# Kernel optimization log

Measured on AMD Instinct MI355X. Metric: run time of the kernel, lower is better.

## Reference

```python
import jax, jax.numpy as jnp
import numpy as np

N, E, G, D = 100000, 400000, 4000, 128
AF, BF, L = 74, 12, 11  # atom/bond feat sizes; L = n_layers-1 GNN layers after GetContext


def _p(k, shape, fan):
    return jax.random.normal(k, shape, dtype=jnp.float32) * (fan ** -0.5)


def setup_inputs() -> dict:
    key = jax.random.key(0)
    ks = iter(jax.random.split(key, 32))
    z = lambda *s: jnp.zeros(s, jnp.float32)
    return dict(
        atom_feats=jax.random.normal(next(ks), (N, AF), jnp.float32),
        bond_feats=jax.random.normal(next(ks), (E, BF), jnp.float32),
        src=jax.random.randint(next(ks), (E,), 0, N, jnp.int32),
        dst=jax.random.randint(next(ks), (E,), 0, N, jnp.int32),
        node_graph_ids=jnp.sort(jax.random.randint(next(ks), (N,), 0, G, jnp.int32)),
        W_node=_p(next(ks), (AF, D), AF), b_node=z(D),
        W_edge1=_p(next(ks), (AF + BF, D), AF + BF), b_edge1=z(D),
        W_edge2=_p(next(ks), (2 * D, 1), 2 * D), b_edge2=z(1),
        W_et=_p(next(ks), (D, D), D), b_et=z(D),
        gru0_Wih=_p(next(ks), (3 * D, D), D), gru0_bih=z(3 * D),
        gru0_Whh=_p(next(ks), (3 * D, D), D), gru0_bhh=z(3 * D),
        Wpe=_p(next(ks), (L, 2 * D, 1), 2 * D), bpe=z(L, 1),
        Wpn=_p(next(ks), (L, D, D), D), bpn=z(L, D),
        gru_Wih=_p(next(ks), (L, 3 * D, D), D), gru_bih=z(L, 3 * D),
        gru_Whh=_p(next(ks), (L, 3 * D, D), D), gru_bhh=z(L, 3 * D),
        Wr1=_p(next(ks), (D, D), D), br1=z(D),
        Wr2=_p(next(ks), (D, D), D), br2=z(D),
    )


def leaky_relu(x):
    return jnp.where(x > 0, x, 0.01 * x)


def edge_softmax(logits, dst):
    # softmax of edge logits grouped by destination node (DGL edge_softmax)
    m = jax.ops.segment_max(logits, dst, num_segments=N)
    m = jnp.where(jnp.isfinite(m), m, 0.0)
    e = jnp.exp(logits - m[dst])
    s = jax.ops.segment_sum(e, dst, num_segments=N)
    return e / s[dst]


def gru_cell(x, h, Wih, bih, Whh, bhh):
    gi = x @ Wih.T + bih
    gh = h @ Whh.T + bhh
    ir, iz, ig = jnp.split(gi, 3, axis=-1)
    hr, hz, hg = jnp.split(gh, 3, axis=-1)
    r = jax.nn.sigmoid(ir + hr)
    z = jax.nn.sigmoid(iz + hz)
    n = jnp.tanh(ig + r * hg)
    return (1.0 - z) * n + z * h


def _attentive_fp(atom_feats, bond_feats, src, dst, node_graph_ids,
                  W_node, b_node, W_edge1, b_edge1, W_edge2, b_edge2,
                  W_et, b_et, gru0_Wih, gru0_bih, gru0_Whh, gru0_bhh,
                  Wpe, bpe, Wpn, bpn, gru_Wih, gru_bih, gru_Whh, gru_bhh,
                  Wr1, br1, Wr2, br2):
    # --- GetContext (dropout = identity at inference) ---
    hv_new = leaky_relu(atom_feats @ W_node + b_node)                       # [N,D]
    he1 = leaky_relu(jnp.concatenate([atom_feats[src], bond_feats], 1) @ W_edge1 + b_edge1)  # [E,D]
    logits = leaky_relu(jnp.concatenate([hv_new[dst], he1], 1) @ W_edge2 + b_edge2)          # [E,1]
    a = edge_softmax(logits, dst)
    c = jax.ops.segment_sum(a * (he1 @ W_et + b_et), dst, num_segments=N)   # [N,D]
    h = jax.nn.relu(gru_cell(jax.nn.elu(c), hv_new, gru0_Wih, gru0_bih, gru0_Whh, gru0_bhh))

    # --- 11 GNNLayers (AttentiveGRU2) via scan over stacked params ---
    def layer(h, p):
        Wpe_l, bpe_l, Wpn_l, bpn_l, Wih, bih, Whh, bhh = p
        lg = leaky_relu(jnp.concatenate([h[dst], h[src]], 1) @ Wpe_l + bpe_l)  # [E,1]
        a = edge_softmax(lg, dst)
        hp = h @ Wpn_l + bpn_l
        c = jax.ops.segment_sum(hp[src] * a, dst, num_segments=N)
        return jax.nn.relu(gru_cell(jax.nn.elu(c), h, Wih, bih, Whh, bhh)), None

    h, _ = jax.lax.scan(layer, h, (Wpe, bpe, Wpn, bpn, gru_Wih, gru_bih, gru_Whh, gru_bhh))

    # --- MLPNodeReadout, mode='mean' ---
    x = jax.nn.relu(h @ Wr1 + br1) @ Wr2 + br2
    sums = jax.ops.segment_sum(x, node_graph_ids, num_segments=G)
    counts = jax.ops.segment_sum(jnp.ones((N, 1), x.dtype), node_graph_ids, num_segments=G)
    return sums / jnp.maximum(counts, 1.0)                                  # [G,D]


def reference(atom_feats, bond_feats, src, dst, node_graph_ids,
              W_node, b_node, W_edge1, b_edge1, W_edge2, b_edge2,
              W_et, b_et, gru0_Wih, gru0_bih, gru0_Whh, gru0_bhh,
              Wpe, bpe, Wpn, bpn, gru_Wih, gru_bih, gru_Whh, gru_bhh,
              Wr1, br1, Wr2, br2):
    return _attentive_fp(atom_feats, bond_feats, src, dst, node_graph_ids,
                         W_node, b_node, W_edge1, b_edge1, W_edge2, b_edge2,
                         W_et, b_et, gru0_Wih, gru0_bih, gru0_Whh, gru0_bhh,
                         Wpe, bpe, Wpn, bpn, gru_Wih, gru_bih, gru_Whh, gru_bhh,
                         Wr1, br1, Wr2, br2)
```

## Files before the change

### kernel.cpp

```cpp
#include <hip/hip_runtime.h>
#include <cstdio>
#include <cstddef>

enum { ACT_NONE = 0, ACT_LEAKY = 1, ACT_RELU = 2 };

typedef __attribute__((ext_vector_type(8))) short short8v;
typedef __attribute__((ext_vector_type(4))) float f32x4;

__device__ __forceinline__ float leakyf(float x) { return x > 0.f ? x : 0.01f * x; }

__device__ __forceinline__ unsigned fenc(float f) {
    unsigned u = __float_as_uint(f);
    return (u & 0x80000000u) ? ~u : (u | 0x80000000u);
}
__device__ __forceinline__ float fdec(unsigned u) {
    return (u & 0x80000000u) ? __uint_as_float(u & 0x7FFFFFFFu) : __uint_as_float(~u);
}

__device__ __forceinline__ unsigned bf16rtn(float x) {
    unsigned u = __float_as_uint(x);
    return (u + 0x7FFFu + ((u >> 16) & 1u)) >> 16;
}
__device__ __forceinline__ void split8(float4 a, float4 b, short8v& hi, short8v& lo) {
    const float v[8] = {a.x, a.y, a.z, a.w, b.x, b.y, b.z, b.w};
#pragma unroll
    for (int i = 0; i < 8; i++) {
        const unsigned hb = bf16rtn(v[i]);
        const float r = v[i] - __uint_as_float(hb << 16);
        hi[i] = (short)hb;
        lo[i] = (short)bf16rtn(r);
    }
}

__global__ __launch_bounds__(256) void wsplit_k(
    const float* __restrict__ Wih, const float* __restrict__ Whh,
    unsigned short* __restrict__ whi, unsigned short* __restrict__ wlo)
{
    const int i4 = (blockIdx.x * 256 + threadIdx.x) * 4;
    if (i4 >= 98304) return;
    const float* src = (i4 < 49152) ? (Wih + i4) : (Whh + (i4 - 49152));
    const float4 v = *(const float4*)src;
    const float vv[4] = {v.x, v.y, v.z, v.w};
    unsigned short h4[4], l4[4];
#pragma unroll
    for (int i = 0; i < 4; i++) {
        const unsigned hb = bf16rtn(vv[i]);
        const float r = vv[i] - __uint_as_float(hb << 16);
        h4[i] = (unsigned short)hb;
        l4[i] = (unsigned short)bf16rtn(r);
    }
    *(ushort4*)&whi[i4] = make_ushort4(h4[0], h4[1], h4[2], h4[3]);
    *(ushort4*)&wlo[i4] = make_ushort4(l4[0], l4[1], l4[2], l4[3]);
}

__global__ __launch_bounds__(256) void wsplitT_k(
    const float* __restrict__ W,
    unsigned short* __restrict__ whi, unsigned short* __restrict__ wlo)
{
    const int idx = blockIdx.x * 256 + threadIdx.x;
    if (idx >= 16384) return;
    const int k = idx >> 7, col = idx & 127;
    const float v = W[idx];
    const unsigned hb = bf16rtn(v);
    const float r = v - __uint_as_float(hb << 16);
    whi[col * 128 + k] = (unsigned short)hb;
    wlo[col * 128 + k] = (unsigned short)bf16rtn(r);
}

__global__ __launch_bounds__(256) void wsplitT96_k(
    const float* __restrict__ W,
    unsigned short* __restrict__ whi, unsigned short* __restrict__ wlo, int K)
{
    const int idx = blockIdx.x * 256 + threadIdx.x;
    if (idx >= 12288) return;
    const int col = idx / 96, k = idx - col * 96;
    const float v = (k < K) ? W[(size_t)k * 128 + col] : 0.f;
    const unsigned hb = bf16rtn(v);
    const float r = v - __uint_as_float(hb << 16);
    whi[idx] = (unsigned short)hb;
    wlo[idx] = (unsigned short)bf16rtn(r);
}

__global__ __launch_bounds__(512) void gru_fused_mfma_k(
    const float* __restrict__ cbuf, const unsigned short* __restrict__ whi,
    const unsigned short* __restrict__ wlo, const float* __restrict__ bih,
    const float* __restrict__ bhh, float* __restrict__ h,
    const float* __restrict__ wa, const float* __restrict__ wb,
    float* __restrict__ pd, float* __restrict__ ps,
    const unsigned short* __restrict__ w3hi, const unsigned short* __restrict__ w3lo,
    const float* __restrict__ b3, float* __restrict__ out3, int act3, int M)
{
    __shared__ __align__(16) char smem[64 * 132 * 4];
    short (*lhi)[4][64][8] = (short(*)[4][64][8])smem;
    short (*llo)[4][64][8] = (short(*)[4][64][8])(smem + 16384);
    float (*fbuf)[132] = (float(*)[132])smem;

    const int t    = threadIdx.x;
    const int lane = t & 63;
    const int w    = t >> 6;
    const int rBase = blockIdx.x * 64;

    const int sRS = t >> 3, sQ = t & 7;
    const int sRow = rBase + sRS;
    const int sRT = sRS >> 4, sLrow = sRS & 15;

    auto stage = [&](const float* __restrict__ A, bool doElu) {
#pragma unroll
        for (int half = 0; half < 2; half++) {
            const int k0 = sQ * 16 + half * 8;
            const int kc = k0 >> 5;
            const int g  = (k0 & 31) >> 3;
            float4 f0 = make_float4(0.f, 0.f, 0.f, 0.f);
            float4 f1 = make_float4(0.f, 0.f, 0.f, 0.f);
            if (sRow < M) {
                f0 = *(const float4*)&A[(size_t)sRow * 128 + k0];
                f1 = *(const float4*)&A[(size_t)sRow * 128 + k0 + 4];
                if (doElu) {
                    f0.x = f0.x > 0.f ? f0.x : expm1f(f0.x);
                    f0.y = f0.y > 0.f ? f0.y : expm1f(f0.y);
                    f0.z = f0.z > 0.f ? f0.z : expm1f(f0.z);
                    f0.w = f0.w > 0.f ? f0.w : expm1f(f0.w);
                    f1.x = f1.x > 0.f ? f1.x : expm1f(f1.x);
                    f1.y = f1.y > 0.f ? f1.y : expm1f(f1.y);
                    f1.z = f1.z > 0.f ? f1.z : expm1f(f1.z);
                    f1.w = f1.w > 0.f ? f1.w : expm1f(f1.w);
                }
            }
            short8v h8, l8;
            split8(f0, f1, h8, l8);
            *(short8v*)&lhi[sRT][kc][sLrow + g * 16][0] = h8;
            *(short8v*)&llo[sRT][kc][sLrow + g * 16][0] = l8;
        }
    };

    f32x4 accr[4], accz[4], accig[4], acchg[4];
#pragma unroll
    for (int rt = 0; rt < 4; rt++) {
        accr[rt]  = (f32x4){0.f, 0.f, 0.f, 0.f};
        accz[rt]  = (f32x4){0.f, 0.f, 0.f, 0.f};
        accig[rt] = (f32x4){0.f, 0.f, 0.f, 0.f};
        acchg[rt] = (f32x4){0.f, 0.f, 0.f, 0.f};
    }

    const int cw   = w * 16 + (lane & 15);
    const int koff = (lane >> 4) * 8;

    stage(cbuf, true);
    __syncthreads();
#pragma unroll
    for (int kc = 0; kc < 4; kc++) {
        short8v bh[3], bl[3];
#pragma unroll
        for (int g = 0; g < 3; g++) {
            const size_t off = (size_t)(g * 128 + cw) * 128 + kc * 32 + koff;
            bh[g] = *(const short8v*)&whi[off];
            bl[g] = *(const short8v*)&wlo[off];
        }
#pragma unroll
        for (int rt = 0; rt < 4; rt++) {
            const short8v ah = *(const short8v*)&lhi[rt][kc][lane][0];
            const short8v al = *(const short8v*)&llo[rt][kc][lane][0];
            accr[rt]  = __builtin_amdgcn_mfma_f32_16x16x32_bf16(ah, bh[0], accr[rt], 0, 0, 0);
            accr[rt]  = __builtin_amdgcn_mfma_f32_16x16x32_bf16(al, bh[0], accr[rt], 0, 0, 0);
            accr[rt]  = __builtin_amdgcn_mfma_f32_16x16x32_bf16(ah, bl[0], accr[rt], 0, 0, 0);
            accz[rt]  = __builtin_amdgcn_mfma_f32_16x16x32_bf16(ah, bh[1], accz[rt], 0, 0, 0);
            accz[rt]  = __builtin_amdgcn_mfma_f32_16x16x32_bf16(al, bh[1], accz[rt], 0, 0, 0);
            accz[rt]  = __builtin_amdgcn_mfma_f32_16x16x32_bf16(ah, bl[1], accz[rt], 0, 0, 0);
            accig[rt] = __builtin_amdgcn_mfma_f32_16x16x32_bf16(ah, bh[2], accig[rt], 0, 0, 0);
            accig[rt] = __builtin_amdgcn_mfma_f32_16x16x32_bf16(al, bh[2], accig[rt], 0, 0, 0);
            accig[rt] = __builtin_amdgcn_mfma_f32_16x16x32_bf16(ah, bl[2], accig[rt], 0, 0, 0);
        }
    }
    __syncthreads();

    stage(h, false);
    __syncthreads();
#pragma unroll
    for (int kc = 0; kc < 4; kc++) {
        short8v bh[3], bl[3];
#pragma unroll
        for (int g = 0; g < 3; g++) {
            const size_t off = (size_t)(384 + g * 128 + cw) * 128 + kc * 32 + koff;
            bh[g] = *(const short8v*)&whi[off];
            bl[g] = *(const short8v*)&wlo[off];
        }
#pragma unroll
        for (int rt = 0; rt < 4; rt++) {
            const short8v ah = *(const short8v*)&lhi[rt][kc][lane][0];
            const short8v al = *(const short8v*)&llo[rt][kc][lane][0];
            accr[rt]  = __builtin_amdgcn_mfma_f32_16x16x32_bf16(ah, bh[0], accr[rt], 0, 0, 0);
            accr[rt]  = __builtin_amdgcn_mfma_f32_16x16x32_bf16(al, bh[0], accr[rt], 0, 0, 0);
            accr[rt]  = __builtin_amdgcn_mfma_f32_16x16x32_bf16(ah, bl[0], accr[rt], 0, 0, 0);
            accz[rt]  = __builtin_amdgcn_mfma_f32_16x16x32_bf16(ah, bh[1], accz[rt], 0, 0, 0);
            accz[rt]  = __builtin_amdgcn_mfma_f32_16x16x32_bf16(al, bh[1], accz[rt], 0, 0, 0);
            accz[rt]  = __builtin_amdgcn_mfma_f32_16x16x32_bf16(ah, bl[1], accz[rt], 0, 0, 0);
            acchg[rt] = __builtin_amdgcn_mfma_f32_16x16x32_bf16(ah, bh[2], acchg[rt], 0, 0, 0);
            acchg[rt] = __builtin_amdgcn_mfma_f32_16x16x32_bf16(al, bh[2], acchg[rt], 0, 0, 0);
            acchg[rt] = __builtin_amdgcn_mfma_f32_16x16x32_bf16(ah, bl[2], acchg[rt], 0, 0, 0);
        }
    }

    const bool post = (wa != nullptr) || (w3hi != nullptr);
    const float br_  = bih[cw] + bhh[cw];
    const float bz_  = bih[128 + cw] + bhh[128 + cw];
    const float big_ = bih[256 + cw];
    const float bhg_ = bhh[256 + cw];
    if (post) __syncthreads();
#pragma unroll
    for (int rt = 0; rt < 4; rt++) {
        const int lr0 = rt * 16 + ((lane >> 4) << 2);
#pragma unroll
        for (int i = 0; i < 4; i++) {
            const int row = rBase + lr0 + i;
            const bool ok = (row < M);
            float hnew = 0.f;
            if (ok) {
                const float hv = h[(size_t)row * 128 + cw];
                const float r  = 1.f / (1.f + expf(-(accr[rt][i] + br_)));
                const float z  = 1.f / (1.f + expf(-(accz[rt][i] + bz_)));
                const float nn = tanhf(accig[rt][i] + big_ + r * (acchg[rt][i] + bhg_));
                hnew = fmaxf((1.f - z) * nn + z * hv, 0.f);
                h[(size_t)row * 128 + cw] = hnew;
            }
            if (post) fbuf[lr0 + i][cw] = hnew;
        }
    }
    if (!post) return;
    __syncthreads();

    if (wa && t < 64 && rBase + t < M) {
        float accd = 0.f, accs = 0.f;
        for (int cc = 0; cc < 128; cc++) {
            const float hv = fbuf[t][cc];
            accd = fmaf(hv, wa[cc], accd);
            accs = fmaf(hv, wb[cc], accs);
        }
        pd[rBase + t] = accd;
        ps[rBase + t] = accs;
    }

    if (w3hi) {
        float4 rv[2][2];
#pragma unroll
        for (int half = 0; half < 2; half++) {
            const int k0 = sQ * 16 + half * 8;
            rv[half][0] = *(const float4*)&fbuf[sRS][k0];
            rv[half][1] = *(const float4*)&fbuf[sRS][k0 + 4];
        }
        __syncthreads();
#pragma unroll
        for (int half = 0; half < 2; half++) {
            const int k0 = sQ * 16 + half * 8;
            const int kc = k0 >> 5;
            const int g  = (k0 & 31) >> 3;
            short8v h8, l8;
            split8(rv[half][0], rv[half][1], h8, l8);
            *(short8v*)&lhi[sRT][kc][sLrow + g * 16][0] = h8;
            *(short8v*)&llo[sRT][kc][sLrow + g * 16][0] = l8;
        }
        __syncthreads();

        f32x4 acc3[4];
#pragma unroll
        for (int rt = 0; rt < 4; rt++) acc3[rt] = (f32x4){0.f, 0.f, 0.f, 0.f};
#pragma unroll
        for (int kc = 0; kc < 4; kc++) {
            const size_t off = (size_t)cw * 128 + kc * 32 + koff;
            const short8v bh = *(const short8v*)&w3hi[off];
            const short8v bl = *(const short8v*)&w3lo[off];
#pragma unroll
            for (int rt = 0; rt < 4; rt++) {
                const short8v ah = *(const short8v*)&lhi[rt][kc][lane][0];
                const short8v al = *(const short8v*)&llo[rt][kc][lane][0];
                acc3[rt] = __builtin_amdgcn_mfma_f32_16x16x32_bf16(ah, bh, acc3[rt], 0, 0, 0);
                acc3[rt] = __builtin_amdgcn_mfma_f32_16x16x32_bf16(al, bh, acc3[rt], 0, 0, 0);
                acc3[rt] = __builtin_amdgcn_mfma_f32_16x16x32_bf16(ah, bl, acc3[rt], 0, 0, 0);
            }
        }
        const float b0 = b3[cw];
#pragma unroll
        for (int rt = 0; rt < 4; rt++) {
            const int r0 = rBase + rt * 16 + ((lane >> 4) << 2);
#pragma unroll
            for (int i = 0; i < 4; i++) {
                const int row = r0 + i;
                if (row >= M) continue;
                float v = acc3[rt][i] + b0;
                if (act3 == ACT_LEAKY)      v = v > 0.f ? v : 0.01f * v;
                else if (act3 == ACT_RELU)  v = fmaxf(v, 0.f);
                out3[(size_t)row * 128 + cw] = v;
            }
        }
    }
}

__global__ __launch_bounds__(512) void mfma128_k(
    const float* __restrict__ A, const unsigned short* __restrict__ whi,
    const unsigned short* __restrict__ wlo, const float* __restrict__ bias,
    float* __restrict__ C, int M, int actOut)
{
    __shared__ short lhi[4][4][64][8];
    __shared__ short llo[4][4][64][8];
    const int t    = threadIdx.x;
    const int lane = t & 63;
    const int w    = t >> 6;
    const int rBase = blockIdx.x * 64;

    {
        const int rS = t >> 3, q = t & 7;
        const int row = rBase + rS;
        const int rt = rS >> 4, lrow = rS & 15;
#pragma unroll
        for (int half = 0; half < 2; half++) {
            const int k0 = q * 16 + half * 8;
            const int kc = k0 >> 5;
            const int g  = (k0 & 31) >> 3;
            float4 f0 = make_float4(0.f, 0.f, 0.f, 0.f);
            float4 f1 = make_float4(0.f, 0.f, 0.f, 0.f);
            if (row < M) {
                f0 = *(const float4*)&A[(size_t)row * 128 + k0];
                f1 = *(const float4*)&A[(size_t)row * 128 + k0 + 4];
            }
            short8v h8, l8;
            split8(f0, f1, h8, l8);
            *(short8v*)&lhi[rt][kc][lrow + g * 16][0] = h8;
            *(short8v*)&llo[rt][kc][lrow + g * 16][0] = l8;
        }
    }
    __syncthreads();

    f32x4 acc[4];
#pragma unroll
    for (int rt = 0; rt < 4; rt++) acc[rt] = (f32x4){0.f, 0.f, 0.f, 0.f};

    const int cw   = w * 16 + (lane & 15);
    const int koff = (lane >> 4) * 8;

#pragma unroll
    for (int kc = 0; kc < 4; kc++) {
        const size_t off = (size_t)cw * 128 + kc * 32 + koff;
        const short8v bh = *(const short8v*)&whi[off];
        const short8v bl = *(const short8v*)&wlo[off];
#pragma unroll
        for (int rt = 0; rt < 4; rt++) {
            const short8v ah = *(const short8v*)&lhi[rt][kc][lane][0];
            const short8v al = *(const short8v*)&llo[rt][kc][lane][0];
            acc[rt] = __builtin_amdgcn_mfma_f32_16x16x32_bf16(ah, bh, acc[rt], 0, 0, 0);
            acc[rt] = __builtin_amdgcn_mfma_f32_16x16x32_bf16(al, bh, acc[rt], 0, 0, 0);
            acc[rt] = __builtin_amdgcn_mfma_f32_16x16x32_bf16(ah, bl, acc[rt], 0, 0, 0);
        }
    }

    const float b0 = bias[cw];
#pragma unroll
    for (int rt = 0; rt < 4; rt++) {
        const int r0 = rBase + rt * 16 + ((lane >> 4) << 2);
#pragma unroll
        for (int i = 0; i < 4; i++) {
            const int row = r0 + i;
            if (row >= M) continue;
            float v = acc[rt][i] + b0;
            if (actOut == ACT_LEAKY)      v = v > 0.f ? v : 0.01f * v;
            else if (actOut == ACT_RELU)  v = fmaxf(v, 0.f);
            C[(size_t)row * 128 + cw] = v;
        }
    }
}

__global__ __launch_bounds__(512) void mfma96_k(
    const float* __restrict__ A1, const float* __restrict__ A2,
    const int* __restrict__ idx,
    const unsigned short* __restrict__ whi, const unsigned short* __restrict__ wlo,
    const float* __restrict__ bias, float* __restrict__ C,
    const float* __restrict__ dotW, float* __restrict__ dotOut,
    int writeC, int M, int K1, int actOut)
{
    __shared__ __align__(16) char smem[64 * 130 * 4];
    short (*lhi)[3][64][8] = (short(*)[3][64][8])smem;
    short (*llo)[3][64][8] = (short(*)[3][64][8])(smem + 12288);
    float (*fbuf)[130] = (float(*)[130])smem;

    const int t    = threadIdx.x;
    const int lane = t & 63;
    const int w    = t >> 6;
    const int rBase = blockIdx.x * 64;

    {
        const int rS = t >> 3, q = t & 7;
        const int row = rBase + rS;
        const int rt = rS >> 4, lrow = rS & 15;
#pragma unroll
        for (int half = 0; half < 2; half++) {
            const int k0 = q * 16 + half * 8;
            if (k0 >= 96) continue;
            const int kc = k0 >> 5;
            const int g  = (k0 & 31) >> 3;
            float v[8] = {0.f, 0.f, 0.f, 0.f, 0.f, 0.f, 0.f, 0.f};
            if (row < M) {
                const int ar = idx ? idx[row] : row;
                const float* __restrict__ a1 = A1 + (size_t)ar * K1;
#pragma unroll
                for (int j = 0; j < 8; j++) {
                    const int k = k0 + j;
                    if (k < K1)                 v[j] = a1[k];
                    else if (A2 && k < K1 + 12) v[j] = A2[(size_t)row * 12 + (k - K1)];
                }
            }
            short8v h8, l8;
            split8(make_float4(v[0], v[1], v[2], v[3]),
                   make_float4(v[4], v[5], v[6], v[7]), h8, l8);
            *(short8v*)&lhi[rt][kc][lrow + g * 16][0] = h8;
            *(short8v*)&llo[rt][kc][lrow + g * 16][0] = l8;
        }
    }
    __syncthreads();

    f32x4 acc[4];
#pragma unroll
    for (int rt = 0; rt < 4; rt++) acc[rt] = (f32x4){0.f, 0.f, 0.f, 0.f};

    const int cw   = w * 16 + (lane & 15);
    const int koff = (lane >> 4) * 8;

#pragma unroll
    for (int kc = 0; kc < 3; kc++) {
        const size_t off = (size_t)cw * 96 + kc * 32 + koff;
        const short8v bh = *(const short8v*)&whi[off];
        const short8v bl = *(const short8v*)&wlo[off];
#pragma unroll
        for (int rt = 0; rt < 4; rt++) {
            const short8v ah = *(const short8v*)&lhi[rt][kc][lane][0];
            const short8v al = *(const short8v*)&llo[rt][kc][lane][0];
            acc[rt] = __builtin_amdgcn_mfma_f32_16x16x32_bf16(ah, bh, acc[rt], 0, 0, 0);
            acc[rt] = __builtin_amdgcn_mfma_f32_16x16x32_bf16(al, bh, acc[rt], 0, 0, 0);
            acc[rt] = __builtin_amdgcn_mfma_f32_16x16x32_bf16(ah, bl, acc[rt], 0, 0, 0);
        }
    }

    const float b0 = bias[cw];
    if (dotOut) __syncthreads();
#pragma unroll
    for (int rt = 0; rt < 4; rt++) {
        const int lr0 = rt * 16 + ((lane >> 4) << 2);
#pragma unroll
        for (int i = 0; i < 4; i++) {
            const int row = rBase + lr0 + i;
            const bool ok = (row < M);
            float v = acc[rt][i] + b0;
            if (actOut == ACT_LEAKY)      v = v > 0.f ? v : 0.01f * v;
            else if (actOut == ACT_RELU)  v = fmaxf(v, 0.f);
            if (ok && writeC) C[(size_t)row * 128 + cw] = v;
            if (dotOut) fbuf[lr0 + i][cw] = ok ? v : 0.f;
        }
    }
    if (dotOut) {
        __syncthreads();
        if (t < 64 && rBase + t < M) {
            float accd = 0.f;
            for (int cc = 0; cc < 128; cc++)
                accd = fmaf(fbuf[t][cc], dotW[cc], accd);
            dotOut[rBase + t] = accd;
        }
    }
}

__global__ __launch_bounds__(256) void edge_lgc_k(
    const float* __restrict__ pd, const float* __restrict__ pe,
    const float* __restrict__ b2, const int* __restrict__ dst,
    float* __restrict__ lg, unsigned* __restrict__ m_u, int E)
{
    const int e = blockIdx.x * blockDim.x + threadIdx.x;
    if (e >= E) return;
    const int d = dst[e];
    const float v = leakyf(pd[d] + pe[e] + b2[0]);
    lg[e] = v;
    atomicMax(&m_u[d], fenc(v));
}

__global__ __launch_bounds__(256) void edge_exp_k(
    float* __restrict__ lg, const unsigned* __restrict__ m_u,
    float* __restrict__ s, const int* __restrict__ dst, int E)
{
    const int e = blockIdx.x * blockDim.x + threadIdx.x;
    if (e >= E) return;
    const int d = dst[e];
    const float ex = expf(lg[e] - fdec(m_u[d]));
    lg[e] = ex;
    atomicAdd(&s[d], ex);
}

__global__ __launch_bounds__(256) void scatter_c_k(
    const float* __restrict__ rows,
    const float* __restrict__ ee, const float* __restrict__ s,
    const int* __restrict__ dst, float* __restrict__ c, int E)
{
    const long long gid = (long long)blockIdx.x * blockDim.x + threadIdx.x;
    const int e = (int)(gid >> 6);
    const int l = (int)(gid & 63);
    if (e >= E) return;
    const int d = dst[e];
    const float a = ee[e] / s[d];
    const float2 v = *(const float2*)&rows[(size_t)e * 128 + l * 2];
    atomicAdd(&c[(size_t)d * 128 + l * 2], a * v.x);
    atomicAdd(&c[(size_t)d * 128 + l * 2 + 1], a * v.y);
}

__global__ __launch_bounds__(256) void hist_k(
    const int* __restrict__ dst, unsigned* __restrict__ cnt, int E)
{
    const int e = blockIdx.x * blockDim.x + threadIdx.x;
    if (e < E) atomicAdd(&cnt[dst[e]], 1u);
}

__global__ __launch_bounds__(1024) void scan_k(
    const unsigned* __restrict__ cnt, int* __restrict__ rp, int N)
{
    __shared__ int wsum[16];
    __shared__ int carry;
    const int t = threadIdx.x, lane = t & 63, wid = t >> 6;
    if (t == 0) carry = 0;
    __syncthreads();
    for (int base = 0; base < N; base += 1024) {
        const int i = base + t;
        const int v = (i < N) ? (int)cnt[i] : 0;
        int x = v;
#pragma unroll
        for (int o = 1; o < 64; o <<= 1) {
            const int y = __shfl_up(x, o, 64);
            if (lane >= o) x += y;
        }
        if (lane == 63) wsum[wid] = x;
        __syncthreads();
        if (wid == 0) {
            const int wv = (lane < 16) ? wsum[lane] : 0;
            int wx = wv;
#pragma unroll
            for (int o = 1; o < 16; o <<= 1) {
                const int y = __shfl_up(wx, o, 64);
                if (lane >= o) wx += y;
            }
            if (lane < 16) wsum[lane] = wx - wv;
        }
        __syncthreads();
        const int excl = carry + wsum[wid] + x - v;
        if (i < N) rp[i] = excl;
        __syncthreads();
        if (t == 1023) carry = excl + v;
        __syncthreads();
    }
    if (t == 0) rp[N] = carry;
}

__global__ __launch_bounds__(256) void fill_csr_k(
    const int* __restrict__ dst, int* __restrict__ pos,
    int* __restrict__ eidx, int E)
{
    const int e = blockIdx.x * blockDim.x + threadIdx.x;
    if (e < E) {
        const int p = atomicAdd(&pos[dst[e]], 1);
        eidx[p] = e;
    }
}

__global__ __launch_bounds__(256) void layer_gather_k(
    const int* __restrict__ rp, const int* __restrict__ eidx,
    const int* __restrict__ src,
    const float* __restrict__ pd, const float* __restrict__ ps,
    const float* __restrict__ bpe,
    const float* __restrict__ hp, float* __restrict__ c, int N)
{
    const int d = blockIdx.x * 4 + (threadIdx.x >> 6);
    const int l = threadIdx.x & 63;
    if (d >= N) return;
    const int beg = rp[d], end = rp[d + 1];
    float acc0 = 0.f, acc1 = 0.f;
    if (beg < end) {
        const float pdd = pd[d];
        const float b   = bpe[0];
        float m = -3.4e38f;
        for (int e = beg + l; e < end; e += 64)
            m = fmaxf(m, leakyf(pdd + ps[src[eidx[e]]] + b));
#pragma unroll
        for (int o = 32; o; o >>= 1) m = fmaxf(m, __shfl_xor(m, o, 64));
        float s = 0.f;
        for (int e = beg + l; e < end; e += 64)
            s += expf(leakyf(pdd + ps[src[eidx[e]]] + b) - m);
#pragma unroll
        for (int o = 32; o; o >>= 1) s += __shfl_xor(s, o, 64);
        const float inv = 1.f / s;
        for (int e = beg; e < end; ++e) {
            const int sr = src[eidx[e]];
            const float a = expf(leakyf(pdd + ps[sr] + b) - m) * inv;
            const float2 v = *(const float2*)&hp[(size_t)sr * 128 + l * 2];
            acc0 = fmaf(a, v.x, acc0);
            acc1 = fmaf(a, v.y, acc1);
        }
    }
    *(float2*)&c[(size_t)d * 128 + l * 2] = make_float2(acc0, acc1);
}

__global__ __launch_bounds__(256) void readout_mean_k(
    const float* __restrict__ x, const int* __restrict__ grp,
    float* __restrict__ out, int G)
{
    const int g = blockIdx.x * 4 + (threadIdx.x >> 6);
    const int l = threadIdx.x & 63;
    if (g >= G) return;
    const int beg = grp[g], end = grp[g + 1];
    float s0 = 0.f, s1 = 0.f;
    for (int r = beg; r < end; ++r) {
        const float2 v = *(const float2*)&x[(size_t)r * 128 + l * 2];
        s0 += v.x;
        s1 += v.y;
    }
    const float inv = 1.f / fmaxf((float)(end - beg), 1.f);
    *(float2*)&out[(size_t)g * 128 + l * 2] = make_float2(s0 * inv, s1 * inv);
}

extern "C" void kernel_launch(void* const* d_in, const int* in_sizes, int n_in,
                              void* d_out, int out_size, void* d_ws, size_t ws_size,
                              hipStream_t stream)
{
    const float* atom   = (const float*)d_in[0];
    const float* bond   = (const float*)d_in[1];
    const int*   src    = (const int*)d_in[2];
    const int*   dst    = (const int*)d_in[3];
    const int*   ngid   = (const int*)d_in[4];
    const float* W_node = (const float*)d_in[5];
    const float* b_node = (const float*)d_in[6];
    const float* W_e1   = (const float*)d_in[7];
    const float* b_e1   = (const float*)d_in[8];
    const float* W_e2   = (const float*)d_in[9];
    const float* b_e2   = (const float*)d_in[10];
    const float* W_et   = (const float*)d_in[11];
    const float* b_et   = (const float*)d_in[12];
    const float* g0_Wih = (const float*)d_in[13];
    const float* g0_bih = (const float*)d_in[14];
    const float* g0_Whh = (const float*)d_in[15];
    const float* g0_bhh = (const float*)d_in[16];
    const float* Wpe    = (const float*)d_in[17];
    const float* bpe    = (const float*)d_in[18];
    const float* Wpn    = (const float*)d_in[19];
    const float* bpn    = (const float*)d_in[20];
    const float* gWih   = (const float*)d_in[21];
    const float* gbih   = (const float*)d_in[22];
    const float* gWhh   = (const float*)d_in[23];
    const float* gbhh   = (const float*)d_in[24];
    const float* Wr1    = (const float*)d_in[25];
    const float* br1    = (const float*)d_in[26];
    const float* Wr2    = (const float*)d_in[27];
    const float* br2    = (const float*)d_in[28];

    const int N = in_sizes[0] / 74;
    const int E = in_sizes[1] / 12;
    const int G = out_size / 128;
    const int L = in_sizes[18];

    char* w = (char*)d_ws;
    auto align256 = [](size_t b) { return (b + 255) & ~(size_t)255; };
    auto alloc = [&](size_t bytes) {
        void* p = (void*)w;
        w += align256(bytes);
        return p;
    };
    float*    h    = (float*)alloc((size_t)N * 128 * 4);
    float*    c    = (float*)alloc((size_t)N * 128 * 4);
    float*    hp   = (float*)alloc((size_t)N * 128 * 4);
    int*      rp   = (int*)alloc((size_t)(N + 1) * 4);
    int*      posb = (int*)alloc((size_t)N * 4);
    int*      eidx = (int*)alloc((size_t)E * 4);
    int*      grp  = (int*)alloc((size_t)(G + 1) * 4);
    unsigned short* gwHi  = (unsigned short*)alloc((size_t)12 * 98304 * 2);
    unsigned short* gwLo  = (unsigned short*)alloc((size_t)12 * 98304 * 2);
    unsigned short* wtHi  = (unsigned short*)alloc((size_t)14 * 16384 * 2);
    unsigned short* wtLo  = (unsigned short*)alloc((size_t)14 * 16384 * 2);
    unsigned short* w96Hi = (unsigned short*)alloc((size_t)2 * 12288 * 2);
    unsigned short* w96Lo = (unsigned short*)alloc((size_t)2 * 12288 * 2);
    float*    pd   = (float*)alloc((size_t)N * 4);
    float*    ps   = (float*)alloc((size_t)N * 4);
    unsigned* m_u  = (unsigned*)alloc((size_t)N * 4);
    float*    sden = (float*)alloc((size_t)N * 4);
    float*    pe   = (float*)alloc((size_t)E * 4);
    float*    lg   = (float*)alloc((size_t)E * 4);
    if ((size_t)(w - (char*)d_ws) > ws_size) {
        fprintf(stderr, "kernel_launch: ws too small: need %zu, have %zu\n",
                (size_t)(w - (char*)d_ws), ws_size);
        return;
    }
    float* out = (float*)d_out;

    const dim3 blk(256);
    auto g64 = [](int M) { return dim3((unsigned)((M + 63) / 64)); };
    const dim3 gEdge((unsigned)((E + 255) / 256));
    const int  Ecap = N;

    wsplit_k<<<dim3(96), blk, 0, stream>>>(g0_Wih, g0_Whh, gwHi, gwLo);
    for (int l = 0; l < L; ++l)
        wsplit_k<<<dim3(96), blk, 0, stream>>>(
            gWih + (size_t)l * 49152, gWhh + (size_t)l * 49152,
            gwHi + (size_t)(l + 1) * 98304, gwLo + (size_t)(l + 1) * 98304);
    for (int l = 0; l < L; ++l)
        wsplitT_k<<<dim3(64), blk, 0, stream>>>(
            Wpn + (size_t)l * 16384, wtHi + (size_t)l * 16384, wtLo + (size_t)l * 16384);
    wsplitT_k<<<dim3(64), blk, 0, stream>>>(W_et, wtHi + (size_t)11 * 16384, wtLo + (size_t)11 * 16384);
    wsplitT_k<<<dim3(64), blk, 0, stream>>>(Wr1,  wtHi + (size_t)12 * 16384, wtLo + (size_t)12 * 16384);
    wsplitT_k<<<dim3(64), blk, 0, stream>>>(Wr2,  wtHi + (size_t)13 * 16384, wtLo + (size_t)13 * 16384);
    wsplitT96_k<<<dim3(48), blk, 0, stream>>>(W_e1,   w96Hi,         w96Lo,         86);
    wsplitT96_k<<<dim3(48), blk, 0, stream>>>(W_node, w96Hi + 12288, w96Lo + 12288, 74);

    auto run_gru = [&](int slot, const float* bih, const float* bhh,
                       const float* wav, const float* wbv,
                       int w3slot, const float* b3, float* out3, int act3) {
        gru_fused_mfma_k<<<g64(N), dim3(512), 0, stream>>>(
            c, gwHi + (size_t)slot * 98304, gwLo + (size_t)slot * 98304,
            bih, bhh, h, wav, wbv, pd, ps,
            wtHi + (size_t)w3slot * 16384, wtLo + (size_t)w3slot * 16384,
            b3, out3, act3, N);
    };
    auto run_mfma128 = [&](const float* A, int slot, const float* bias,
                           float* C, int act) {
        mfma128_k<<<g64(N), dim3(512), 0, stream>>>(
            A, wtHi + (size_t)slot * 16384, wtLo + (size_t)slot * 16384, bias, C, N, act);
    };

    hipMemsetAsync(m_u, 0, (size_t)N * 4, stream);
    hist_k<<<gEdge, blk, 0, stream>>>(dst, m_u, E);
    scan_k<<<dim3(1), dim3(1024), 0, stream>>>(m_u, rp, N);
    hipMemcpyAsync(posb, rp, (size_t)N * 4, hipMemcpyDeviceToDevice, stream);
    fill_csr_k<<<gEdge, blk, 0, stream>>>(dst, posb, eidx, E);
    hipMemsetAsync(m_u, 0, (size_t)G * 4, stream);
    hist_k<<<dim3((unsigned)((N + 255) / 256)), blk, 0, stream>>>(ngid, m_u, N);
    scan_k<<<dim3(1), dim3(1024), 0, stream>>>(m_u, grp, G);

    mfma96_k<<<g64(N), dim3(512), 0, stream>>>(
        atom, nullptr, nullptr, w96Hi + 12288, w96Lo + 12288, b_node, h,
        W_e2, pd, 1, N, 74, ACT_LEAKY);
    for (int base = 0; base < E; base += Ecap) {
        const int ec = (E - base) < Ecap ? (E - base) : Ecap;
        mfma96_k<<<g64(ec), dim3(512), 0, stream>>>(
            atom, bond + (size_t)base * 12, src + base, w96Hi, w96Lo, b_e1,
            nullptr, W_e2 + 128, pe + base, 0, ec, 74, ACT_LEAKY);
    }
    hipMemsetAsync(m_u, 0, (size_t)N * 4, stream);
    hipMemsetAsync(sden, 0, (size_t)N * 4, stream);
    edge_lgc_k<<<gEdge, blk, 0, stream>>>(pd, pe, b_e2, dst, lg, m_u, E);
    edge_exp_k<<<gEdge, blk, 0, stream>>>(lg, m_u, sden, dst, E);
    hipMemsetAsync(c, 0, (size_t)N * 128 * 4, stream);
    for (int base = 0; base < E; base += Ecap) {
        const int ec = (E - base) < Ecap ? (E - base) : Ecap;
        mfma96_k<<<g64(ec), dim3(512), 0, stream>>>(
            atom, bond + (size_t)base * 12, src + base, w96Hi, w96Lo, b_e1,
            hp, nullptr, nullptr, 1, ec, 74, ACT_LEAKY);
        scatter_c_k<<<dim3((unsigned)(((long long)ec * 64 + 255) / 256)), blk, 0, stream>>>(
            hp, lg + base, sden, dst + base, c, ec);
    }
    run_mfma128(c, 11, b_et, c, ACT_NONE);
    run_gru(0, g0_bih, g0_bhh, Wpe, Wpe + 128, 0, bpn, hp, ACT_NONE);

    for (int l = 0; l < L; ++l) {
        layer_gather_k<<<dim3((unsigned)((N + 3) / 4)), blk, 0, stream>>>(
            rp, eidx, src, pd, ps, bpe + l, hp, c, N);
        const bool more = (l + 1 < L);
        if (more) {
            run_gru(l + 1, gbih + (size_t)l * 384, gbhh + (size_t)l * 384,
                    Wpe + (size_t)(l + 1) * 256, Wpe + (size_t)(l + 1) * 256 + 128,
                    l + 1, bpn + (size_t)(l + 1) * 128, hp, ACT_NONE);
        } else {
            run_gru(l + 1, gbih + (size_t)l * 384, gbhh + (size_t)l * 384,
                    nullptr, nullptr, 12, br1, c, ACT_RELU);
        }
    }

    run_mfma128(c, 13, br2, hp, ACT_NONE);
    readout_mean_k<<<dim3((unsigned)((G + 3) / 4)), blk, 0, stream>>>(hp, grp, out, G);

    (void)n_in;
}
```

Measured before the change: 3.770 ms.

## Fuse edge scatter into edge GEMM epilogue and merge weight-split kernels

The edge projection GEMM now applies the softmax weight and atomically accumulates into the destination context buffer directly in its epilogue. This removes the intermediate per-edge hidden buffer write and the separate scatter kernel pass. The chunked loops over edges become single launches, and about 30 small weight-split launches are merged into one kernel. In exchange, atomics are issued per element from the MFMA output layout rather than as coalesced float2 pairs, which could change atomic contention and coalescing.

```diff
diff --git a/kernel.cpp b/kernel.cpp
--- a/kernel.cpp
+++ b/kernel.cpp
@@ -32,53 +32,63 @@
     }
 }
 
-__global__ __launch_bounds__(256) void wsplit_k(
-    const float* __restrict__ Wih, const float* __restrict__ Whh,
-    unsigned short* __restrict__ whi, unsigned short* __restrict__ wlo)
-{
-    const int i4 = (blockIdx.x * 256 + threadIdx.x) * 4;
-    if (i4 >= 98304) return;
-    const float* src = (i4 < 49152) ? (Wih + i4) : (Whh + (i4 - 49152));
-    const float4 v = *(const float4*)src;
-    const float vv[4] = {v.x, v.y, v.z, v.w};
-    unsigned short h4[4], l4[4];
-#pragma unroll
-    for (int i = 0; i < 4; i++) {
-        const unsigned hb = bf16rtn(vv[i]);
-        const float r = vv[i] - __uint_as_float(hb << 16);
-        h4[i] = (unsigned short)hb;
-        l4[i] = (unsigned short)bf16rtn(r);
-    }
-    *(ushort4*)&whi[i4] = make_ushort4(h4[0], h4[1], h4[2], h4[3]);
-    *(ushort4*)&wlo[i4] = make_ushort4(l4[0], l4[1], l4[2], l4[3]);
-}
-
-__global__ __launch_bounds__(256) void wsplitT_k(
-    const float* __restrict__ W,
-    unsigned short* __restrict__ whi, unsigned short* __restrict__ wlo)
-{
-    const int idx = blockIdx.x * 256 + threadIdx.x;
-    if (idx >= 16384) return;
-    const int k = idx >> 7, col = idx & 127;
-    const float v = W[idx];
-    const unsigned hb = bf16rtn(v);
-    const float r = v - __uint_as_float(hb << 16);
-    whi[col * 128 + k] = (unsigned short)hb;
-    wlo[col * 128 + k] = (unsigned short)bf16rtn(r);
-}
-
-__global__ __launch_bounds__(256) void wsplitT96_k(
-    const float* __restrict__ W,
-    unsigned short* __restrict__ whi, unsigned short* __restrict__ wlo, int K)
-{
-    const int idx = blockIdx.x * 256 + threadIdx.x;
-    if (idx >= 12288) return;
-    const int col = idx / 96, k = idx - col * 96;
-    const float v = (k < K) ? W[(size_t)k * 128 + col] : 0.f;
-    const unsigned hb = bf16rtn(v);
-    const float r = v - __uint_as_float(hb << 16);
-    whi[idx] = (unsigned short)hb;
-    wlo[idx] = (unsigned short)bf16rtn(r);
+__global__ __launch_bounds__(256) void wsplit_all_k(
+    const float* __restrict__ g0_Wih, const float* __restrict__ g0_Whh,
+    const float* __restrict__ gWih,   const float* __restrict__ gWhh,
+    const float* __restrict__ Wpn,    const float* __restrict__ W_et,
+    const float* __restrict__ Wr1,    const float* __restrict__ Wr2,
+    const float* __restrict__ W_e1,   const float* __restrict__ W_node,
+    unsigned short* __restrict__ gwHi, unsigned short* __restrict__ gwLo,
+    unsigned short* __restrict__ wtHi, unsigned short* __restrict__ wtLo,
+    unsigned short* __restrict__ w96Hi, unsigned short* __restrict__ w96Lo)
+{
+    const int b = blockIdx.x, t = threadIdx.x;
+    if (b < 1152) {
+        const int slot = b / 96, inner = b % 96;
+        const int i4 = (inner * 256 + t) * 4;
+        if (i4 >= 98304) return;
+        const float* Wih = slot == 0 ? g0_Wih : gWih + (size_t)(slot - 1) * 49152;
+        const float* Whh = slot == 0 ? g0_Whh : gWhh + (size_t)(slot - 1) * 49152;
+        const float* src = (i4 < 49152) ? (Wih + i4) : (Whh + (i4 - 49152));
+        const float4 v = *(const float4*)src;
+        const float vv[4] = {v.x, v.y, v.z, v.w};
+        unsigned short h4[4], l4[4];
+#pragma unroll
+        for (int i = 0; i < 4; i++) {
+            const unsigned hb = bf16rtn(vv[i]);
+            const float r = vv[i] - __uint_as_float(hb << 16);
+            h4[i] = (unsigned short)hb;
+            l4[i] = (unsigned short)bf16rtn(r);
+        }
+        *(ushort4*)&gwHi[(size_t)slot * 98304 + i4] = make_ushort4(h4[0], h4[1], h4[2], h4[3]);
+        *(ushort4*)&gwLo[(size_t)slot * 98304 + i4] = make_ushort4(l4[0], l4[1], l4[2], l4[3]);
+    } else if (b < 2048) {
+        const int q = b - 1152;
+        const int slot = q / 64, inner = q % 64;
+        const int idx = inner * 256 + t;
+        if (idx >= 16384) return;
+        const float* W = slot < 11 ? Wpn + (size_t)slot * 16384
+                        : slot == 11 ? W_et : slot == 12 ? Wr1 : Wr2;
+        const int k = idx >> 7, col = idx & 127;
+        const float v = W[idx];
+        const unsigned hb = bf16rtn(v);
+        const float r = v - __uint_as_float(hb << 16);
+        wtHi[(size_t)slot * 16384 + col * 128 + k] = (unsigned short)hb;
+        wtLo[(size_t)slot * 16384 + col * 128 + k] = (unsigned short)bf16rtn(r);
+    } else {
+        const int q = b - 2048;
+        const int slot = q / 48, inner = q % 48;
+        const int idx = inner * 256 + t;
+        if (idx >= 12288) return;
+        const float* W = slot == 0 ? W_e1 : W_node;
+        const int K   = slot == 0 ? 86 : 74;
+        const int col = idx / 96, k = idx - col * 96;
+        const float v = (k < K) ? W[(size_t)k * 128 + col] : 0.f;
+        const unsigned hb = bf16rtn(v);
+        const float r = v - __uint_as_float(hb << 16);
+        w96Hi[(size_t)slot * 12288 + idx] = (unsigned short)hb;
+        w96Lo[(size_t)slot * 12288 + idx] = (unsigned short)bf16rtn(r);
+    }
 }
 
 __global__ __launch_bounds__(512) void gru_fused_mfma_k(
@@ -373,6 +383,8 @@
     const unsigned short* __restrict__ whi, const unsigned short* __restrict__ wlo,
     const float* __restrict__ bias, float* __restrict__ C,
     const float* __restrict__ dotW, float* __restrict__ dotOut,
+    const float* __restrict__ ee, const float* __restrict__ sd,
+    const int* __restrict__ dstI, float* __restrict__ cAtom,
     int writeC, int M, int K1, int actOut)
 {
     __shared__ __align__(16) char smem[64 * 130 * 4];
@@ -450,6 +462,11 @@
             if (actOut == ACT_LEAKY)      v = v > 0.f ? v : 0.01f * v;
             else if (actOut == ACT_RELU)  v = fmaxf(v, 0.f);
             if (ok && writeC) C[(size_t)row * 128 + cw] = v;
+            if (ok && ee) {
+                const int d = dstI[row];
+                const float a = ee[row] / sd[d];
+                atomicAdd(&cAtom[(size_t)d * 128 + cw], a * v);
+            }
             if (dotOut) fbuf[lr0 + i][cw] = ok ? v : 0.f;
         }
     }
@@ -487,22 +504,6 @@
     const float ex = expf(lg[e] - fdec(m_u[d]));
     lg[e] = ex;
     atomicAdd(&s[d], ex);
-}
-
-__global__ __launch_bounds__(256) void scatter_c_k(
-    const float* __restrict__ rows,
-    const float* __restrict__ ee, const float* __restrict__ s,
-    const int* __restrict__ dst, float* __restrict__ c, int E)
-{
-    const long long gid = (long long)blockIdx.x * blockDim.x + threadIdx.x;
-    const int e = (int)(gid >> 6);
-    const int l = (int)(gid & 63);
-    if (e >= E) return;
-    const int d = dst[e];
-    const float a = ee[e] / s[d];
-    const float2 v = *(const float2*)&rows[(size_t)e * 128 + l * 2];
-    atomicAdd(&c[(size_t)d * 128 + l * 2], a * v.x);
-    atomicAdd(&c[(size_t)d * 128 + l * 2 + 1], a * v.y);
 }
 
 __global__ __launch_bounds__(256) void hist_k(
@@ -692,21 +693,10 @@
     const dim3 blk(256);
     auto g64 = [](int M) { return dim3((unsigned)((M + 63) / 64)); };
     const dim3 gEdge((unsigned)((E + 255) / 256));
-    const int  Ecap = N;
-
-    wsplit_k<<<dim3(96), blk, 0, stream>>>(g0_Wih, g0_Whh, gwHi, gwLo);
-    for (int l = 0; l < L; ++l)
-        wsplit_k<<<dim3(96), blk, 0, stream>>>(
-            gWih + (size_t)l * 49152, gWhh + (size_t)l * 49152,
-            gwHi + (size_t)(l + 1) * 98304, gwLo + (size_t)(l + 1) * 98304);
-    for (int l = 0; l < L; ++l)
-        wsplitT_k<<<dim3(64), blk, 0, stream>>>(
-            Wpn + (size_t)l * 16384, wtHi + (size_t)l * 16384, wtLo + (size_t)l * 16384);
-    wsplitT_k<<<dim3(64), blk, 0, stream>>>(W_et, wtHi + (size_t)11 * 16384, wtLo + (size_t)11 * 16384);
-    wsplitT_k<<<dim3(64), blk, 0, stream>>>(Wr1,  wtHi + (size_t)12 * 16384, wtLo + (size_t)12 * 16384);
-    wsplitT_k<<<dim3(64), blk, 0, stream>>>(Wr2,  wtHi + (size_t)13 * 16384, wtLo + (size_t)13 * 16384);
-    wsplitT96_k<<<dim3(48), blk, 0, stream>>>(W_e1,   w96Hi,         w96Lo,         86);
-    wsplitT96_k<<<dim3(48), blk, 0, stream>>>(W_node, w96Hi + 12288, w96Lo + 12288, 74);
+
+    wsplit_all_k<<<dim3(2144), blk, 0, stream>>>(
+        g0_Wih, g0_Whh, gWih, gWhh, Wpn, W_et, Wr1, Wr2, W_e1, W_node,
+        gwHi, gwLo, wtHi, wtLo, w96Hi, w96Lo);
 
     auto run_gru = [&](int slot, const float* bih, const float* bhh,
                        const float* wav, const float* wbv,
@@ -734,26 +724,18 @@
 
     mfma96_k<<<g64(N), dim3(512), 0, stream>>>(
         atom, nullptr, nullptr, w96Hi + 12288, w96Lo + 12288, b_node, h,
-        W_e2, pd, 1, N, 74, ACT_LEAKY);
-    for (int base = 0; base < E; base += Ecap) {
-        const int ec = (E - base) < Ecap ? (E - base) : Ecap;
-        mfma96_k<<<g64(ec), dim3(512), 0, stream>>>(
-            atom, bond + (size_t)base * 12, src + base, w96Hi, w96Lo, b_e1,
-            nullptr, W_e2 + 128, pe + base, 0, ec, 74, ACT_LEAKY);
-    }
+        W_e2, pd, nullptr, nullptr, nullptr, nullptr, 1, N, 74, ACT_LEAKY);
+    mfma96_k<<<g64(E), dim3(512), 0, stream>>>(
+        atom, bond, src, w96Hi, w96Lo, b_e1,
+        nullptr, W_e2 + 128, pe, nullptr, nullptr, nullptr, nullptr, 0, E, 74, ACT_LEAKY);
     hipMemsetAsync(m_u, 0, (size_t)N * 4, stream);
     hipMemsetAsync(sden, 0, (size_t)N * 4, stream);
     edge_lgc_k<<<gEdge, blk, 0, stream>>>(pd, pe, b_e2, dst, lg, m_u, E);
     edge_exp_k<<<gEdge, blk, 0, stream>>>(lg, m_u, sden, dst, E);
     hipMemsetAsync(c, 0, (size_t)N * 128 * 4, stream);
-    for (int base = 0; base < E; base += Ecap) {
-        const int ec = (E - base) < Ecap ? (E - base) : Ecap;
-        mfma96_k<<<g64(ec), dim3(512), 0, stream>>>(
-            atom, bond + (size_t)base * 12, src + base, w96Hi, w96Lo, b_e1,
-            hp, nullptr, nullptr, 1, ec, 74, ACT_LEAKY);
-        scatter_c_k<<<dim3((unsigned)(((long long)ec * 64 + 255) / 256)), blk, 0, stream>>>(
-            hp, lg + base, sden, dst + base, c, ec);
-    }
+    mfma96_k<<<g64(E), dim3(512), 0, stream>>>(
+        atom, bond, src, w96Hi, w96Lo, b_e1,
+        nullptr, nullptr, nullptr, lg, sden, dst, c, 0, E, 74, ACT_LEAKY);
     run_mfma128(c, 11, b_et, c, ACT_NONE);
     run_gru(0, g0_bih, g0_bhh, Wpe, Wpe + 128, 0, bpn, hp, ACT_NONE);
 
```

Result: faster. 3.505 ms (-7.0%).
